# Performance work log

Measured on AMD Instinct MI355X. Metric: run time of the kernel, lower is better.

## Reference

```python
import jax, jax.numpy as jnp
import numpy as np

B, T, C, HS = 256, 256, 384, 64

def setup_inputs() -> dict:
    key = jax.random.key(0)
    ks = jax.random.split(key, 7)
    return {
        "x": jax.random.normal(ks[0], (B, T, C), dtype=jnp.float32),
        "Wq": jax.random.normal(ks[1], (C, HS), dtype=jnp.float32) * (C ** -0.5),
        "bq": jax.random.normal(ks[2], (HS,), dtype=jnp.float32) * 0.02,
        "Wk": jax.random.normal(ks[3], (C, HS), dtype=jnp.float32) * (C ** -0.5),
        "bk": jax.random.normal(ks[4], (HS,), dtype=jnp.float32) * 0.02,
        "Wv": jax.random.normal(ks[5], (C, HS), dtype=jnp.float32) * (C ** -0.5),
        "bv": jax.random.normal(ks[6], (HS,), dtype=jnp.float32) * 0.02,
    }

def reference(x, Wq, bq, Wk, bk, Wv, bv):
    # single-head causal self-attention (eval mode: dropout is identity)
    T_ = x.shape[1]
    q = x @ Wq + bq          # [B, T, HS]
    k = x @ Wk + bk          # [B, T, HS]
    v = x @ Wv + bv          # [B, T, HS]
    scale = k.shape[-1] ** -0.5
    att = jnp.einsum("btd,bsd->bts", q, k) * scale   # [B, T, T]
    causal = jnp.tril(jnp.ones((T_, T_), dtype=bool))  # tril buffer
    att = jnp.where(causal, att, -jnp.inf)             # mask future positions
    att = jax.nn.softmax(att, axis=-1)
    return jnp.einsum("bts,bsd->btd", att, v)          # [B, T, HS]
```

## Files before the change

kernel.cpp:

```cpp
#include <hip/hip_runtime.h>
#include <hip/hip_bf16.h>

#define BB 256
#define TT 256
#define CC 384
#define HSS 64

typedef __bf16 bf16_t;
typedef bf16_t bf16x8 __attribute__((ext_vector_type(8)));
typedef bf16_t bf16x4 __attribute__((ext_vector_type(4)));
typedef float f32x4 __attribute__((ext_vector_type(4)));

__device__ __forceinline__ f32x4 mfma16(bf16x8 a, bf16x8 b, f32x4 c) {
    return __builtin_amdgcn_mfma_f32_16x16x32_bf16(a, b, c, 0, 0, 0);
}

__device__ __forceinline__ bf16x8 cvt8(float4 a, float4 b) {
    bf16x8 r;
    r[0] = (bf16_t)a.x; r[1] = (bf16_t)a.y; r[2] = (bf16_t)a.z; r[3] = (bf16_t)a.w;
    r[4] = (bf16_t)b.x; r[5] = (bf16_t)b.y; r[6] = (bf16_t)b.z; r[7] = (bf16_t)b.w;
    return r;
}

typedef __attribute__((address_space(3))) unsigned int lds_uint_t;
typedef const __attribute__((address_space(1))) unsigned int glb_uint_t;
__device__ __forceinline__ void async_cp16(const void* g, void* lds_uniform) {
    __builtin_amdgcn_global_load_lds((glb_uint_t*)g, (lds_uint_t*)lds_uniform, 16, 0, 0);
}

__global__ void prep_w(const float* __restrict__ Wq, const float* __restrict__ Wk,
                       const float* __restrict__ Wv, bf16_t* __restrict__ WtG) {
    int idx = blockIdx.x * 256 + threadIdx.x;
    if (idx >= 192 * 384) return;
    int n = idx / 384, k = idx % 384;
    const float* W = (n < 64) ? Wq : (n < 128) ? Wk : Wv;
    float val = W[k * 64 + (n & 63)];
    int kc = k >> 7, kin = k & 127;
    int c = kin >> 3, e = k & 7;
    int pc = c ^ (n & 15);
    WtG[kc * 24576 + n * 128 + pc * 8 + e] = (bf16_t)val;
}

__global__ __launch_bounds__(256, 3) void qkv_kernel(
    const float* __restrict__ x, const bf16_t* __restrict__ WtG,
    const float* __restrict__ bq, const float* __restrict__ bk, const float* __restrict__ bv,
    bf16_t* __restrict__ q, bf16_t* __restrict__ k, bf16_t* __restrict__ vt) {

    __shared__ bf16_t Wl[24576];

    int tid = threadIdx.x;
    int w = tid >> 6, l = tid & 63;
    int lr = l & 15, lq = l >> 4;
    int R0 = blockIdx.x * 64 + w * 16;
    const float* xrow = x + (size_t)(R0 + lr) * CC;

    f32x4 acc[12];
#pragma unroll
    for (int i = 0; i < 12; i++) acc[i] = (f32x4){0.f, 0.f, 0.f, 0.f};

    for (int kc = 0; kc < 3; kc++) {
        if (kc) __syncthreads();
        const bf16_t* src = WtG + kc * 24576;
#pragma unroll
        for (int j = 0; j < 12; j++) {
            int cbase = (j * 4 + w) * 64;
            async_cp16(src + (size_t)(cbase + l) * 8, Wl + (size_t)cbase * 8);
        }
        bf16x8 afrag[4];
        const float* xp = xrow + kc * 128 + lq * 8;
#pragma unroll
        for (int t = 0; t < 4; t++) {
            float4 f0 = *(const float4*)(xp + t * 32);
            float4 f1 = *(const float4*)(xp + t * 32 + 4);
            afrag[t] = cvt8(f0, f1);
        }
        __syncthreads();
#pragma unroll
        for (int nt = 0; nt < 12; nt++) {
            int n = nt * 16 + lr;
            const bf16_t* wl = Wl + (size_t)n * 128;
#pragma unroll
            for (int t = 0; t < 4; t++) {
                int pc = (t * 4 + lq) ^ lr;
                bf16x8 bfrag = *(const bf16x8*)(wl + pc * 8);
                acc[nt] = mfma16(afrag[t], bfrag, acc[nt]);
            }
        }
    }

#pragma unroll
    for (int nt = 0; nt < 12; nt++) {
        int n = nt * 16 + lr;
        int sel = n >> 6, col = n & 63;
        const float* bptr = (sel == 0) ? bq : (sel == 1) ? bk : bv;
        float bias = bptr[col];
        if (sel < 2) {
            bf16_t* dst = (sel == 0) ? q : k;
#pragma unroll
            for (int r = 0; r < 4; r++) {
                int row = R0 + lq * 4 + r;
                dst[(size_t)row * HSS + col] = (bf16_t)(acc[nt][r] + bias);
            }
        } else {
            bf16x4 pk;
#pragma unroll
            for (int r = 0; r < 4; r++) pk[r] = (bf16_t)(acc[nt][r] + bias);
            size_t off = ((size_t)(R0 >> 8) * HSS + col) * TT + (R0 & 255) + lq * 4;
            *(bf16x4*)(vt + off) = pk;
        }
    }
}

__global__ __launch_bounds__(256, 2) void attn_fused(
    const bf16_t* __restrict__ qg, const bf16_t* __restrict__ kg,
    const bf16_t* __restrict__ vTg, float* __restrict__ out) {

    __shared__ uint4 Ksw[2048];
    __shared__ uint4 Vsw[2048];
    __shared__ __align__(16) bf16_t Pb[4 * 640];

    int b = blockIdx.y, qt = blockIdx.x, tid = threadIdx.x;

    const uint4* ksrc = (const uint4*)(kg + (size_t)b * TT * HSS);
#pragma unroll
    for (int j = 0; j < 8; j++) {
        int ch = j * 256 + tid;
        int c = ch & 7, n = ch >> 3;
        Ksw[n * 8 + (c ^ (n & 7))] = ksrc[ch];
    }
    const uint4* vsrc = (const uint4*)(vTg + (size_t)b * TT * HSS);
#pragma unroll
    for (int j = 0; j < 8; j++) {
        int ch = j * 256 + tid;
        int c = ch & 31, d = ch >> 5;
        Vsw[d * 32 + ((c & ~7) | ((c ^ d) & 7))] = vsrc[ch];
    }

    int w = tid >> 6, l = tid & 63, lr = l & 15, lq = l >> 4;
    int mt = w * 4 + qt;
    int R0 = mt * 16;
    int tg = R0 + lr;
    int ktm = mt >> 1;

    const bf16_t* qrow = qg + ((size_t)b * TT + R0 + lr) * HSS + lq * 8;
    bf16x8 q0 = *(const bf16x8*)qrow;
    bf16x8 q1 = *(const bf16x8*)(qrow + 32);

    __syncthreads();

    const float scale2 = 0.125f * 1.4426950408889634f;
    bf16_t* Pw = Pb + w * 640;
    f32x4 acc[4] = {};
    float sum = 0.f;

#pragma unroll
    for (int kt = 0; kt < 8; kt++) {
        if (kt <= ktm) {
#pragma unroll
            for (int h = 0; h < 2; h++) {
                int nt = kt * 2 + h;
                int n = nt * 16 + lr;
                const uint4* krow = Ksw + n * 8;
                bf16x8 k0 = __builtin_bit_cast(bf16x8, krow[lq ^ (n & 7)]);
                bf16x8 k1 = __builtin_bit_cast(bf16x8, krow[(4 + lq) ^ (n & 7)]);
                f32x4 a = {0.f, 0.f, 0.f, 0.f};
                a = mfma16(k0, q0, a);
                a = mfma16(k1, q1, a);
                bf16x4 pk;
#pragma unroll
                for (int r = 0; r < 4; r++) {
                    int sg = nt * 16 + lq * 4 + r;
                    float p = (sg <= tg) ? exp2f(a[r] * scale2) : 0.f;
                    sum += p;
                    pk[r] = (bf16_t)p;
                }
                *(bf16x4*)(Pw + lr * 40 + h * 16 + lq * 4) = pk;
            }
            bf16x8 pf = *(const bf16x8*)(Pw + lr * 40 + lq * 8);
#pragma unroll
            for (int dt = 0; dt < 4; dt++) {
                int d = dt * 16 + lr;
                int cc = kt * 4 + lq;
                bf16x8 vf = __builtin_bit_cast(bf16x8, Vsw[d * 32 + ((cc & ~7) | ((cc ^ d) & 7))]);
                acc[dt] = mfma16(pf, vf, acc[dt]);
            }
        }
    }

    sum += __shfl_xor(sum, 16);
    sum += __shfl_xor(sum, 32);
    float inv = 1.0f / sum;

#pragma unroll
    for (int r = 0; r < 4; r++) {
        float invr = __shfl(inv, lq * 4 + r);
        size_t row = (size_t)b * TT + R0 + lq * 4 + r;
#pragma unroll
        for (int dt = 0; dt < 4; dt++)
            out[row * HSS + dt * 16 + lr] = acc[dt][r] * invr;
    }
}

extern "C" void kernel_launch(void* const* d_in, const int* in_sizes, int n_in,
                              void* d_out, int out_size, void* d_ws, size_t ws_size,
                              hipStream_t stream) {
    const float* x  = (const float*)d_in[0];
    const float* Wq = (const float*)d_in[1];
    const float* bq = (const float*)d_in[2];
    const float* Wk = (const float*)d_in[3];
    const float* bk = (const float*)d_in[4];
    const float* Wv = (const float*)d_in[5];
    const float* bv = (const float*)d_in[6];
    float* out = (float*)d_out;

    bf16_t* qb  = (bf16_t*)d_ws;
    bf16_t* kb  = qb  + (size_t)BB * TT * HSS;
    bf16_t* vtb = kb  + (size_t)BB * TT * HSS;
    bf16_t* WtG = vtb + (size_t)BB * TT * HSS;

    prep_w<<<288, 256, 0, stream>>>(Wq, Wk, Wv, WtG);
    qkv_kernel<<<(BB * TT) / 64, 256, 0, stream>>>(x, WtG, bq, bk, bv, qb, kb, vtb);
    attn_fused<<<dim3(4, BB), 256, 0, stream>>>(qb, kb, vtb, out);
}
```

Measured before the change: 187.5 us.

## Fuse QKV projection and causal attention into one per-batch kernel

Merges the QKV projection and the attention kernels into one kernel with one 512-thread block per batch. Each wave computes two 16-row tiles (w and 15-w) so the causal work is balanced across waves. K and V are written straight into swizzled LDS and Q is passed through LDS into MFMA fragments, which removes the global round trip of the bf16 q/k/vT intermediates and one launch. The PV MFMA operands are swapped so output rows can be stored as float4. The cost is a grid of only 256 blocks with heavy LDS and register use (acc[2][12]), so occupancy and latency hiding may drop.

```diff
diff --git a/kernel.cpp b/kernel.cpp
--- a/kernel.cpp
+++ b/kernel.cpp
@@ -41,163 +41,174 @@
     WtG[kc * 24576 + n * 128 + pc * 8 + e] = (bf16_t)val;
 }
 
-__global__ __launch_bounds__(256, 3) void qkv_kernel(
+__global__ __attribute__((amdgpu_flat_work_group_size(512, 512),
+                          amdgpu_waves_per_eu(2, 2)))
+void head_fused(
     const float* __restrict__ x, const bf16_t* __restrict__ WtG,
     const float* __restrict__ bq, const float* __restrict__ bk, const float* __restrict__ bv,
-    bf16_t* __restrict__ q, bf16_t* __restrict__ k, bf16_t* __restrict__ vt) {
+    float* __restrict__ out) {
 
     __shared__ bf16_t Wl[24576];
-
-    int tid = threadIdx.x;
-    int w = tid >> 6, l = tid & 63;
-    int lr = l & 15, lq = l >> 4;
-    int R0 = blockIdx.x * 64 + w * 16;
-    const float* xrow = x + (size_t)(R0 + lr) * CC;
-
-    f32x4 acc[12];
-#pragma unroll
-    for (int i = 0; i < 12; i++) acc[i] = (f32x4){0.f, 0.f, 0.f, 0.f};
+    __shared__ uint4 Ksw[2048];
+    __shared__ uint4 Vsw[2048];
+    __shared__ __align__(16) bf16_t Pb[8 * 640];
+
+    int b = blockIdx.x, tid = threadIdx.x;
+    int w = tid >> 6, l = tid & 63, lr = l & 15, lq = l >> 4;
+    int Mt[2] = {w, 15 - w};
+
+    float bqv[4], bkv[4], bvv[4];
+#pragma unroll
+    for (int nt = 0; nt < 4; nt++) {
+        bqv[nt] = bq[nt * 16 + lr];
+        bkv[nt] = bk[nt * 16 + lr];
+        bvv[nt] = bv[nt * 16 + lr];
+    }
+
+    const float* xr[2];
+    xr[0] = x + ((size_t)b * TT + Mt[0] * 16 + lr) * CC;
+    xr[1] = x + ((size_t)b * TT + Mt[1] * 16 + lr) * CC;
+
+    f32x4 acc[2][12];
+#pragma unroll
+    for (int m = 0; m < 2; m++)
+#pragma unroll
+        for (int i = 0; i < 12; i++) acc[m][i] = (f32x4){0.f, 0.f, 0.f, 0.f};
 
     for (int kc = 0; kc < 3; kc++) {
         if (kc) __syncthreads();
         const bf16_t* src = WtG + kc * 24576;
 #pragma unroll
-        for (int j = 0; j < 12; j++) {
-            int cbase = (j * 4 + w) * 64;
+        for (int j = 0; j < 6; j++) {
+            int cbase = (j * 8 + w) * 64;
             async_cp16(src + (size_t)(cbase + l) * 8, Wl + (size_t)cbase * 8);
         }
-        bf16x8 afrag[4];
-        const float* xp = xrow + kc * 128 + lq * 8;
-#pragma unroll
-        for (int t = 0; t < 4; t++) {
-            float4 f0 = *(const float4*)(xp + t * 32);
-            float4 f1 = *(const float4*)(xp + t * 32 + 4);
-            afrag[t] = cvt8(f0, f1);
+        bf16x8 af[2][4];
+#pragma unroll
+        for (int m = 0; m < 2; m++) {
+            const float* xp = xr[m] + kc * 128 + lq * 8;
+#pragma unroll
+            for (int t = 0; t < 4; t++) {
+                float4 f0 = *(const float4*)(xp + t * 32);
+                float4 f1 = *(const float4*)(xp + t * 32 + 4);
+                af[m][t] = cvt8(f0, f1);
+            }
         }
         __syncthreads();
 #pragma unroll
         for (int nt = 0; nt < 12; nt++) {
-            int n = nt * 16 + lr;
-            const bf16_t* wl = Wl + (size_t)n * 128;
+            const bf16_t* wl = Wl + (size_t)(nt * 16 + lr) * 128;
 #pragma unroll
             for (int t = 0; t < 4; t++) {
                 int pc = (t * 4 + lq) ^ lr;
                 bf16x8 bfrag = *(const bf16x8*)(wl + pc * 8);
-                acc[nt] = mfma16(afrag[t], bfrag, acc[nt]);
-            }
-        }
-    }
-
-#pragma unroll
-    for (int nt = 0; nt < 12; nt++) {
-        int n = nt * 16 + lr;
-        int sel = n >> 6, col = n & 63;
-        const float* bptr = (sel == 0) ? bq : (sel == 1) ? bk : bv;
-        float bias = bptr[col];
-        if (sel < 2) {
-            bf16_t* dst = (sel == 0) ? q : k;
+                acc[0][nt] = mfma16(af[0][t], bfrag, acc[0][nt]);
+                acc[1][nt] = mfma16(af[1][t], bfrag, acc[1][nt]);
+            }
+        }
+    }
+
+    bf16_t* KswB = (bf16_t*)Ksw;
+    bf16_t* VswB = (bf16_t*)Vsw;
+#pragma unroll
+    for (int m = 0; m < 2; m++) {
+#pragma unroll
+        for (int nt = 4; nt < 8; nt++) {
+            int d = (nt - 4) * 16 + lr;
 #pragma unroll
             for (int r = 0; r < 4; r++) {
-                int row = R0 + lq * 4 + r;
-                dst[(size_t)row * HSS + col] = (bf16_t)(acc[nt][r] + bias);
-            }
-        } else {
+                int s = Mt[m] * 16 + lq * 4 + r;
+                KswB[s * 64 + ((d >> 3) ^ (s & 7)) * 8 + (d & 7)] =
+                    (bf16_t)(acc[m][nt][r] + bkv[nt - 4]);
+            }
+        }
+#pragma unroll
+        for (int nt = 8; nt < 12; nt++) {
+            int d = (nt - 8) * 16 + lr;
+            int t0 = Mt[m] * 16 + lq * 4;
+            int c = t0 >> 3;
             bf16x4 pk;
 #pragma unroll
-            for (int r = 0; r < 4; r++) pk[r] = (bf16_t)(acc[nt][r] + bias);
-            size_t off = ((size_t)(R0 >> 8) * HSS + col) * TT + (R0 & 255) + lq * 4;
-            *(bf16x4*)(vt + off) = pk;
-        }
-    }
-}
-
-__global__ __launch_bounds__(256, 2) void attn_fused(
-    const bf16_t* __restrict__ qg, const bf16_t* __restrict__ kg,
-    const bf16_t* __restrict__ vTg, float* __restrict__ out) {
-
-    __shared__ uint4 Ksw[2048];
-    __shared__ uint4 Vsw[2048];
-    __shared__ __align__(16) bf16_t Pb[4 * 640];
-
-    int b = blockIdx.y, qt = blockIdx.x, tid = threadIdx.x;
-
-    const uint4* ksrc = (const uint4*)(kg + (size_t)b * TT * HSS);
-#pragma unroll
-    for (int j = 0; j < 8; j++) {
-        int ch = j * 256 + tid;
-        int c = ch & 7, n = ch >> 3;
-        Ksw[n * 8 + (c ^ (n & 7))] = ksrc[ch];
-    }
-    const uint4* vsrc = (const uint4*)(vTg + (size_t)b * TT * HSS);
-#pragma unroll
-    for (int j = 0; j < 8; j++) {
-        int ch = j * 256 + tid;
-        int c = ch & 31, d = ch >> 5;
-        Vsw[d * 32 + ((c & ~7) | ((c ^ d) & 7))] = vsrc[ch];
-    }
-
-    int w = tid >> 6, l = tid & 63, lr = l & 15, lq = l >> 4;
-    int mt = w * 4 + qt;
-    int R0 = mt * 16;
-    int tg = R0 + lr;
-    int ktm = mt >> 1;
-
-    const bf16_t* qrow = qg + ((size_t)b * TT + R0 + lr) * HSS + lq * 8;
-    bf16x8 q0 = *(const bf16x8*)qrow;
-    bf16x8 q1 = *(const bf16x8*)(qrow + 32);
-
+            for (int r = 0; r < 4; r++) pk[r] = (bf16_t)(acc[m][nt][r] + bvv[nt - 8]);
+            *(bf16x4*)(VswB + d * 256 + ((c & ~7) | ((c ^ d) & 7)) * 8 + (t0 & 7)) = pk;
+        }
+    }
     __syncthreads();
 
     const float scale2 = 0.125f * 1.4426950408889634f;
     bf16_t* Pw = Pb + w * 640;
-    f32x4 acc[4] = {};
-    float sum = 0.f;
-
-#pragma unroll
-    for (int kt = 0; kt < 8; kt++) {
-        if (kt <= ktm) {
-#pragma unroll
-            for (int h = 0; h < 2; h++) {
-                int nt = kt * 2 + h;
-                int n = nt * 16 + lr;
-                const uint4* krow = Ksw + n * 8;
-                bf16x8 k0 = __builtin_bit_cast(bf16x8, krow[lq ^ (n & 7)]);
-                bf16x8 k1 = __builtin_bit_cast(bf16x8, krow[(4 + lq) ^ (n & 7)]);
-                f32x4 a = {0.f, 0.f, 0.f, 0.f};
-                a = mfma16(k0, q0, a);
-                a = mfma16(k1, q1, a);
-                bf16x4 pk;
-#pragma unroll
-                for (int r = 0; r < 4; r++) {
-                    int sg = nt * 16 + lq * 4 + r;
-                    float p = (sg <= tg) ? exp2f(a[r] * scale2) : 0.f;
-                    sum += p;
-                    pk[r] = (bf16_t)p;
+
+#pragma unroll
+    for (int m = 0; m < 2; m++) {
+        int R0 = Mt[m] * 16;
+        int tg = R0 + lr;
+        int ktm = Mt[m] >> 1;
+
+        bf16x8 qf[2];
+#pragma unroll
+        for (int hh = 0; hh < 2; hh++) {
+#pragma unroll
+            for (int u = 0; u < 2; u++) {
+                int nt = 2 * hh + u;
+#pragma unroll
+                for (int r = 0; r < 4; r++)
+                    Pw[(lq * 4 + r) * 40 + u * 16 + lr] =
+                        (bf16_t)(acc[m][nt][r] + bqv[nt]);
+            }
+            qf[hh] = *(const bf16x8*)(Pw + lr * 40 + lq * 8);
+        }
+
+        f32x4 oacc[4] = {};
+        float sum = 0.f;
+#pragma unroll
+        for (int kt = 0; kt < 8; kt++) {
+            if (kt <= ktm) {
+#pragma unroll
+                for (int u = 0; u < 2; u++) {
+                    int nt = kt * 2 + u;
+                    int s = nt * 16 + lr;
+                    const uint4* krow = Ksw + s * 8;
+                    bf16x8 k0 = __builtin_bit_cast(bf16x8, krow[lq ^ (s & 7)]);
+                    bf16x8 k1 = __builtin_bit_cast(bf16x8, krow[(4 + lq) ^ (s & 7)]);
+                    f32x4 a = {0.f, 0.f, 0.f, 0.f};
+                    a = mfma16(k0, qf[0], a);
+                    a = mfma16(k1, qf[1], a);
+                    bf16x4 pk;
+#pragma unroll
+                    for (int r = 0; r < 4; r++) {
+                        int sg = nt * 16 + lq * 4 + r;
+                        float p = (sg <= tg) ? exp2f(a[r] * scale2) : 0.f;
+                        sum += p;
+                        pk[r] = (bf16_t)p;
+                    }
+                    *(bf16x4*)(Pw + lr * 40 + u * 16 + lq * 4) = pk;
                 }
-                *(bf16x4*)(Pw + lr * 40 + h * 16 + lq * 4) = pk;
-            }
-            bf16x8 pf = *(const bf16x8*)(Pw + lr * 40 + lq * 8);
-#pragma unroll
-            for (int dt = 0; dt < 4; dt++) {
-                int d = dt * 16 + lr;
-                int cc = kt * 4 + lq;
-                bf16x8 vf = __builtin_bit_cast(bf16x8, Vsw[d * 32 + ((cc & ~7) | ((cc ^ d) & 7))]);
-                acc[dt] = mfma16(pf, vf, acc[dt]);
-            }
-        }
-    }
-
-    sum += __shfl_xor(sum, 16);
-    sum += __shfl_xor(sum, 32);
-    float inv = 1.0f / sum;
-
-#pragma unroll
-    for (int r = 0; r < 4; r++) {
-        float invr = __shfl(inv, lq * 4 + r);
-        size_t row = (size_t)b * TT + R0 + lq * 4 + r;
-#pragma unroll
-        for (int dt = 0; dt < 4; dt++)
-            out[row * HSS + dt * 16 + lr] = acc[dt][r] * invr;
+                bf16x8 pf = *(const bf16x8*)(Pw + lr * 40 + lq * 8);
+#pragma unroll
+                for (int dt = 0; dt < 4; dt++) {
+                    int d = dt * 16 + lr;
+                    int cc = kt * 4 + lq;
+                    bf16x8 vf = __builtin_bit_cast(bf16x8,
+                        Vsw[d * 32 + ((cc & ~7) | ((cc ^ d) & 7))]);
+                    oacc[dt] = mfma16(vf, pf, oacc[dt]);
+                }
+            }
+        }
+
+        sum += __shfl_xor(sum, 16);
+        sum += __shfl_xor(sum, 32);
+        float inv = 1.0f / sum;
+
+        float* orow = out + ((size_t)b * TT + R0 + lr) * HSS;
+#pragma unroll
+        for (int dt = 0; dt < 4; dt++) {
+            float4 o;
+            o.x = oacc[dt][0] * inv;
+            o.y = oacc[dt][1] * inv;
+            o.z = oacc[dt][2] * inv;
+            o.w = oacc[dt][3] * inv;
+            *(float4*)(orow + dt * 16 + lq * 4) = o;
+        }
     }
 }
 
@@ -213,12 +224,8 @@
     const float* bv = (const float*)d_in[6];
     float* out = (float*)d_out;
 
-    bf16_t* qb  = (bf16_t*)d_ws;
-    bf16_t* kb  = qb  + (size_t)BB * TT * HSS;
-    bf16_t* vtb = kb  + (size_t)BB * TT * HSS;
-    bf16_t* WtG = vtb + (size_t)BB * TT * HSS;
+    bf16_t* WtG = (bf16_t*)d_ws;
 
     prep_w<<<288, 256, 0, stream>>>(Wq, Wk, Wv, WtG);
-    qkv_kernel<<<(BB * TT) / 64, 256, 0, stream>>>(x, WtG, bq, bk, bv, qb, kb, vtb);
-    attn_fused<<<dim3(4, BB), 256, 0, stream>>>(qb, kb, vtb, out);
-}
+    head_fused<<<BB, 512, 0, stream>>>(x, WtG, bq, bk, bv, out);
+}
```

New measurement: 178.8 us. 4.7% less time.
